# Optimization experiments

Measured on AMD Instinct MI355X. Metric: run time of the kernel, lower is better.

Reference implementation:

```python
import jax, jax.numpy as jnp
import numpy as np

N, C, T, V, K, COUT, H, DK, DV = 32, 64, 512, 25, 3, 64, 4, 16, 16
BN_EPS = 1e-5
LN_EPS = 1e-6


def setup_inputs() -> dict:
    key = jax.random.key(0)
    ks = jax.random.split(key, 8)
    s = jnp.float32(0.02)
    f32 = jnp.float32
    inp = {
        'x': jax.random.normal(ks[0], (N, C, T, V), f32),
        'A': jax.random.uniform(ks[1], (K, V, V), f32) / V,
        # BatchNorm2d(in_channels) -- eval mode params
        'bn1_g': jnp.ones((C,), f32), 'bn1_b': jnp.zeros((C,), f32),
        'bn1_m': jnp.zeros((C,), f32), 'bn1_v': jnp.ones((C,), f32),
        # partconv: Conv2d(C, COUT*K, kernel (1,1)) == pointwise
        'pconv_w': jax.random.normal(ks[2], (K * COUT, C), f32) * s,
        'pconv_b': jnp.zeros((K * COUT,), f32),
        # AdapGraphConv projections (stored as [d_in, d_out] for x @ W)
        'wq': jax.random.normal(ks[3], (C, H * DK), f32) * s,
        'wk': jax.random.normal(ks[4], (C, H * DK), f32) * s,
        'wv': jax.random.normal(ks[5], (C, H * DV), f32) * s,
        'fc_w': jax.random.normal(ks[6], (H * DV, COUT), f32) * s,
        'ln_g': jnp.ones((C,), f32), 'ln_b': jnp.zeros((C,), f32),
        # weighted-sum gate scalar
        'gate_w': jnp.float32(1.0),
        # SCN output BN
        'bn2_g': jnp.ones((COUT,), f32), 'bn2_b': jnp.zeros((COUT,), f32),
        'bn2_m': jnp.zeros((COUT,), f32), 'bn2_v': jnp.ones((COUT,), f32),
        # TCN: Conv2d(COUT, COUT, (9,1), padding (4,0))
        'tconv_w': jax.random.normal(ks[7], (COUT, COUT, 9, 1), f32) * s,
        'tconv_b': jnp.zeros((COUT,), f32),
        'bn3_g': jnp.ones((COUT,), f32), 'bn3_b': jnp.zeros((COUT,), f32),
        'bn3_m': jnp.zeros((COUT,), f32), 'bn3_v': jnp.ones((COUT,), f32),
    }
    return inp


def _bn(x, g, b, m, v):
    # eval-mode BatchNorm2d over channel axis 1 of NCHW
    sh = (1, -1, 1, 1)
    inv = g.reshape(sh) / jnp.sqrt(v.reshape(sh) + BN_EPS)
    return (x - m.reshape(sh)) * inv + b.reshape(sh)


def _block(x, A, bn1_g, bn1_b, bn1_m, bn1_v, pconv_w, pconv_b, wq, wk, wv,
           fc_w, ln_g, ln_b, gate_w, bn2_g, bn2_b, bn2_m, bn2_v,
           tconv_w, tconv_b, bn3_g, bn3_b, bn3_m, bn3_v):
    n, c, t, v = x.shape
    inp = _bn(x, bn1_g, bn1_b, bn1_m, bn1_v)                 # [N,C,T,V]
    # pointwise partconv then partition-wise graph aggregation
    f_c = jnp.einsum('nctv,oc->notv', inp, pconv_w) + pconv_b.reshape(1, -1, 1, 1)
    f_c = f_c.reshape(n, K, COUT, t, v)
    f_c = jnp.einsum('nkctv,kvw->nctw', f_c, A)              # [N,COUT,T,V]
    # AdapGraphConv over joints, batched across N*T
    fa = inp.transpose(0, 2, 3, 1).reshape(n * t, v, c)      # [NT,V,C]
    mu = fa.mean(-1, keepdims=True)
    var = fa.var(-1, keepdims=True)
    qn = (fa - mu) / jnp.sqrt(var + LN_EPS) * ln_g + ln_b    # LN on q only
    q = (qn @ wq).reshape(n * t, v, H, DK)
    k = (fa @ wk).reshape(n * t, v, H, DK)
    vv = (fa @ wv).reshape(n * t, v, H, DV)
    att = jnp.einsum('bqhd,bkhd->bhqk', q, k) / np.float32(np.sqrt(DK))
    att = jax.nn.softmax(att, axis=-1)                       # [NT,H,V,V]
    xh = jnp.einsum('bhqk,bkhd->bqhd', att, vv).reshape(n * t, v, H * DV)
    fa_out = xh @ fc_w + fa                                  # identity residual (C==COUT)
    fa_out = fa_out.reshape(n, t, v, COUT).transpose(0, 3, 1, 2)
    # gated fusion, BN + ReLU
    f = (fa_out * gate_w + f_c) * 0.5
    f = jax.nn.relu(_bn(f, bn2_g, bn2_b, bn2_m, bn2_v))
    # temporal conv (9,1), pad (4,0), then BN; dropout=0 => identity
    y = jax.lax.conv_general_dilated(
        f, tconv_w, window_strides=(1, 1), padding=((4, 4), (0, 0)),
        dimension_numbers=('NCHW', 'OIHW', 'NCHW'))
    y = y + tconv_b.reshape(1, -1, 1, 1)
    y = _bn(y, bn3_g, bn3_b, bn3_m, bn3_v)
    return jax.nn.relu(y + x)                                # identity block residual


def reference(x, A, bn1_g, bn1_b, bn1_m, bn1_v, pconv_w, pconv_b, wq, wk, wv,
              fc_w, ln_g, ln_b, gate_w, bn2_g, bn2_b, bn2_m, bn2_v,
              tconv_w, tconv_b, bn3_g, bn3_b, bn3_m, bn3_v):
    return _block(x, A, bn1_g, bn1_b, bn1_m, bn1_v, pconv_w, pconv_b, wq, wk,
                  wv, fc_w, ln_g, ln_b, gate_w, bn2_g, bn2_b, bn2_m, bn2_v,
                  tconv_w, tconv_b, bn3_g, bn3_b, bn3_m, bn3_v)
```

## Files before the change

### kernel.cpp

```cpp
#include <hip/hip_runtime.h>

#define NB   32
#define C    64
#define T    512
#define V    25
#define KP   3
#define CO   64
#define H    4
#define BN_EPS 1e-5f
#define LN_EPS 1e-6f

typedef float f32x4 __attribute__((ext_vector_type(4)));
typedef short bf16x8 __attribute__((ext_vector_type(8)));
typedef unsigned short u16;
typedef unsigned int u32;
typedef u32 u32x2 __attribute__((ext_vector_type(2)));
#define MFMA(a,b,c) __builtin_amdgcn_mfma_f32_16x16x32_bf16((a),(b),(c),0,0,0)

__device__ __forceinline__ u16 f2bf(float x) {
    union { float f; unsigned u; } v; v.f = x;
    unsigned r = (v.u + 0x7FFFu + ((v.u >> 16) & 1u)) >> 16;
    return (u16)r;
}
__device__ __forceinline__ float bf2f(u16 h) {
    union { unsigned u; float f; } v; v.u = ((unsigned)h) << 16;
    return v.f;
}
__device__ __forceinline__ u32x2 pack4(const f32x4& a) {
    u32x2 p;
    p[0] = (u32)f2bf(a[0]) | ((u32)f2bf(a[1]) << 16);
    p[1] = (u32)f2bf(a[2]) | ((u32)f2bf(a[3]) << 16);
    return p;
}

#define WOFF 52428800ull

__global__ __launch_bounds__(256) void prep_kernel(
    const float* __restrict__ A, const float* __restrict__ pconv_w,
    const float* __restrict__ pconv_b,
    const float* __restrict__ wq, const float* __restrict__ wk,
    const float* __restrict__ wv, const float* __restrict__ fc_w,
    const float* __restrict__ tconv_w, const float* __restrict__ tconv_b,
    const float* __restrict__ ln_g, const float* __restrict__ ln_b,
    const float* __restrict__ bn1_g, const float* __restrict__ bn1_b,
    const float* __restrict__ bn1_m, const float* __restrict__ bn1_v,
    const float* __restrict__ bn2_g, const float* __restrict__ bn2_b,
    const float* __restrict__ bn2_m, const float* __restrict__ bn2_v,
    const float* __restrict__ bn3_g, const float* __restrict__ bn3_b,
    const float* __restrict__ bn3_m, const float* __restrict__ bn3_v,
    u16* __restrict__ akt, u16* __restrict__ wp2,
    u16* __restrict__ wqt, u16* __restrict__ wkt, u16* __restrict__ wvt,
    u16* __restrict__ fct, float* __restrict__ bagg, u16* __restrict__ wtc,
    float* __restrict__ uvec, float* __restrict__ w0vec,
    float* __restrict__ bnc)
{
    const int stride = gridDim.x * 256;
    for (int i = blockIdx.x * 256 + threadIdx.x; i < 71296; i += stride) {
        if (i < 3840) {
            int k = i / 1280, r = i - k * 1280, w = r / 40, v = r - w * 40;
            float val = (w < V && v < V) ? A[k * V * V + v * V + w] : 0.f;
            akt[i] = f2bf(val);
        } else if (i < 16128) {
            int i2 = i - 3840;
            int c = i2 / 192, kk = i2 - c * 192, k = kk / 64, ci = kk - k * 64;
            wp2[i2] = f2bf(pconv_w[(k * 64 + c) * 64 + ci]);
        } else if (i < 20224) {
            int i2 = i - 16128; int j = i2 / 64, c = i2 - j * 64;
            wqt[i2] = f2bf(wq[c * 64 + j] * ln_g[c]);
        } else if (i < 24320) {
            int i2 = i - 20224; int j = i2 / 64, c = i2 - j * 64;
            wkt[i2] = f2bf(wk[c * 64 + j]);
        } else if (i < 28416) {
            int i2 = i - 24320; int j = i2 / 64, c = i2 - j * 64;
            wvt[i2] = f2bf(wv[c * 64 + j]);
        } else if (i < 32512) {
            int i2 = i - 28416; int c = i2 / 64, d = i2 - c * 64;
            fct[i2] = f2bf(fc_w[d * 64 + c]);
        } else if (i < 34112) {
            int i2 = i - 32512; int c = i2 / 25, w = i2 - c * 25;
            float s = 0.f;
            for (int k = 0; k < KP; ++k) {
                float cs = 0.f;
                for (int v = 0; v < V; ++v) cs += A[k * V * V + v * V + w];
                s += pconv_b[k * 64 + c] * cs;
            }
            bagg[i2] = s;
        } else if (i < 70976) {
            int i2 = i - 34112;
            int co = i2 / 576, rem = i2 - co * 576, dt = rem / 64, ci = rem - dt * 64;
            wtc[i2] = f2bf(tconv_w[(co * 64 + ci) * 9 + dt]);
        } else if (i < 71040) {
            int j = i - 70976; float s = 0.f;
            for (int c = 0; c < 64; ++c) s += ln_g[c] * wq[c * 64 + j];
            uvec[j] = s;
        } else if (i < 71104) {
            int j = i - 71040; float s = 0.f;
            for (int c = 0; c < 64; ++c) s += ln_b[c] * wq[c * 64 + j];
            w0vec[j] = s;
        } else if (i < 71168) {
            int c = i - 71104;
            float s1 = bn1_g[c] * rsqrtf(bn1_v[c] + BN_EPS);
            bnc[c]      = s1;
            bnc[64 + c] = bn1_b[c] - bn1_m[c] * s1;
        } else if (i < 71232) {
            int c = i - 71168;
            float s2 = bn2_g[c] * rsqrtf(bn2_v[c] + BN_EPS);
            bnc[128 + c] = s2;
            bnc[192 + c] = bn2_b[c] - bn2_m[c] * s2;
        } else {
            int c = i - 71232;
            float s3 = bn3_g[c] * rsqrtf(bn3_v[c] + BN_EPS);
            bnc[256 + c] = s3;
            bnc[320 + c] = tconv_b[c] * s3 + (bn3_b[c] - bn3_m[c] * s3);
        }
    }
}

#define OFF_INPV  0
#define OFF_XHT   0
#define OFF_INPT  5120
#define OFF_Q2    8720
#define OFF_ATT   8720
#define OFF_K2    15520
#define OFF_VVT   22320
#define OFF_LNS   27440
#define OFF_MU    29040
#define OFF_RSTD  29140
#define OFF_YT    29240
#define OFF_S     29240
#define LDS_BYTES 39640

#define LDSF(off) ((float*)(s_raw + (off)))
#define LDSH(off) ((u16*)(s_raw + (off)))
#define LDSV8(b)  (*(const bf16x8*)(s_raw + (b)))

__global__ __launch_bounds__(256) void scn_kernel(
    const float* __restrict__ x,
    const u16* __restrict__ akt, const u16* __restrict__ wp2,
    const u16* __restrict__ wqt, const u16* __restrict__ wkt,
    const u16* __restrict__ wvt, const u16* __restrict__ fct,
    const float* __restrict__ bagg,
    const float* __restrict__ uvec, const float* __restrict__ w0vec,
    const float* __restrict__ gate_w, const float* __restrict__ bnc,
    u16* __restrict__ f_out)
{
    const int nt   = blockIdx.x;
    const int n    = nt >> 9;
    const int t    = nt & 511;
    const int tid  = threadIdx.x;
    const int lane = tid & 63;
    const int wid  = tid >> 6;
    const int r0   = lane & 15;
    const int g    = lane >> 4;

    __shared__ __align__(16) unsigned char s_raw[LDS_BYTES];

    const float gate = gate_w[0];

    #pragma unroll
    for (int it = 0; it < 7; ++it) {
        int i = tid + it * 256;
        if (i < 1600) {
            int c = i / 25, v = i - c * 25;
            float f = x[((n * 64 + c) * 512 + t) * 25 + v] * bnc[c] + bnc[64 + c];
            u16 hb = f2bf(f);
            LDSH(OFF_INPV)[c * 40 + v] = hb;
            LDSH(OFF_INPT)[v * 72 + c] = hb;
        }
    }
    for (int i = tid; i < 960; i += 256) {
        int c = i / 15, vz = 25 + (i - c * 15);
        LDSH(OFF_INPV)[c * 40 + vz] = 0;
    }
    {
        bf16x8 z = {0,0,0,0,0,0,0,0};
        for (int i = tid; i < 1170; i += 256)
            *(bf16x8*)(s_raw + OFF_Q2 + i * 16) = z;
    }
    __syncthreads();

    #pragma unroll
    for (int ii = 0; ii < 6; ++ii) {
        int idx = wid * 6 + ii;
        int k = idx >> 3, rem = idx & 7, mt = rem >> 1, ntt = rem & 1;
        bf16x8 a = LDSV8(OFF_INPV + ((mt * 16 + r0) * 40 + g * 8) * 2);
        bf16x8 b = *(const bf16x8*)(&akt[(k * 32 + ntt * 16 + r0) * 40 + g * 8]);
        f32x4 acc = {0.f, 0.f, 0.f, 0.f};
        acc = MFMA(a, b, acc);
        int w = ntt * 16 + r0, cb = mt * 16 + g * 4;
        if (w < 25)
            *(u32x2*)&LDSH(OFF_YT)[w * 200 + k * 64 + cb] = pack4(acc);
    }
    #pragma unroll
    for (int ii = 0; ii < 2; ++ii) {
        int idx = wid * 2 + ii, mtj = idx >> 1, ntv = idx & 1;
        f32x4 acc = {0.f, 0.f, 0.f, 0.f};
        #pragma unroll
        for (int ks = 0; ks < 2; ++ks) {
            bf16x8 a = *(const bf16x8*)(&wkt[(mtj * 16 + r0) * 64 + ks * 32 + g * 8]);
            bf16x8 b = LDSV8(OFF_INPT + ((ntv * 16 + r0) * 72 + ks * 32 + g * 8) * 2);
            acc = MFMA(a, b, acc);
        }
        int v = ntv * 16 + r0;
        if (v < 25)
            *(u32x2*)&LDSH(OFF_K2)[v * 136 + mtj * 32 + g * 4] = pack4(acc);
    }
    #pragma unroll
    for (int ii = 0; ii < 2; ++ii) {
        int idx = wid * 2 + ii, mt = idx >> 2, ntt = idx & 3;
        f32x4 acc = {0.f, 0.f, 0.f, 0.f};
        #pragma unroll
        for (int ks = 0; ks < 2; ++ks) {
            bf16x8 a = LDSV8(OFF_INPT + ((mt * 16 + r0) * 72 + ks * 32 + g * 8) * 2);
            bf16x8 b = *(const bf16x8*)(&wvt[(ntt * 16 + r0) * 64 + ks * 32 + g * 8]);
            acc = MFMA(a, b, acc);
        }
        int j = ntt * 16 + r0;
        #pragma unroll
        for (int r = 0; r < 4; ++r) {
            int v = mt * 16 + g * 4 + r;
            if (v < 25) LDSH(OFF_VVT)[j * 40 + v] = f2bf(acc[r]);
        }
    }
    #pragma unroll
    for (int ii = 0; ii < 2; ++ii) {
        int idx = wid * 2 + ii, mtj = idx >> 1, ntv = idx & 1;
        f32x4 acc = {0.f, 0.f, 0.f, 0.f};
        #pragma unroll
        for (int ks = 0; ks < 2; ++ks) {
            bf16x8 a = *(const bf16x8*)(&wqt[(mtj * 16 + r0) * 64 + ks * 32 + g * 8]);
            bf16x8 b = LDSV8(OFF_INPT + ((ntv * 16 + r0) * 72 + ks * 32 + g * 8) * 2);
            acc = MFMA(a, b, acc);
        }
        int v = ntv * 16 + r0;
        if (v < 25)
            *(u32x2*)&LDSH(OFF_Q2)[v * 136 + mtj * 32 + g * 4] = pack4(acc);
    }
    if (tid < 200) {
        int v = tid >> 3, p = tid & 7;
        const u16* row = LDSH(OFF_INPT) + v * 72 + p * 8;
        float s1 = 0.f, s2 = 0.f;
        #pragma unroll
        for (int cc = 0; cc < 8; ++cc) {
            float xv = bf2f(row[cc]);
            s1 += xv; s2 += xv * xv;
        }
        LDSF(OFF_LNS)[(v * 8 + p) * 2]     = s1;
        LDSF(OFF_LNS)[(v * 8 + p) * 2 + 1] = s2;
    }
    __syncthreads();

    if (tid < 25) {
        float s1 = 0.f, s2 = 0.f;
        #pragma unroll
        for (int p = 0; p < 8; ++p) {
            s1 += LDSF(OFF_LNS)[(tid * 8 + p) * 2];
            s2 += LDSF(OFF_LNS)[(tid * 8 + p) * 2 + 1];
        }
        float mu = s1 * (1.f / 64.f);
        float var = s2 * (1.f / 64.f) - mu * mu;
        LDSF(OFF_MU)[tid]   = mu;
        LDSF(OFF_RSTD)[tid] = rsqrtf(var + LN_EPS);
    }
    __syncthreads();

    #pragma unroll
    for (int it = 0; it < 7; ++it) {
        int i = tid + it * 256;
        if (i < 1600) {
            int v = i >> 6, j = i & 63;
            int jo = (j >> 4) * 32 + (j & 15);
            float raw = bf2f(LDSH(OFF_Q2)[v * 136 + jo]);
            float rs = LDSF(OFF_RSTD)[v], m = LDSF(OFF_MU)[v];
            LDSH(OFF_Q2)[v * 136 + jo] =
                f2bf(0.25f * (rs * raw - rs * m * uvec[j] + w0vec[j]));
        }
    }
    f32x4 agg_reg[2];
    #pragma unroll
    for (int ii = 0; ii < 2; ++ii) {
        int idx = wid * 2 + ii, mt = idx >> 1, ntt = idx & 1;
        f32x4 acc = {0.f, 0.f, 0.f, 0.f};
        #pragma unroll
        for (int ks = 0; ks < 6; ++ks) {
            bf16x8 a = *(const bf16x8*)(&wp2[(mt * 16 + r0) * 192 + ks * 32 + g * 8]);
            int brow = ntt * 16 + r0; if (brow > 24) brow = 24;
            bf16x8 b = LDSV8(OFF_YT + (brow * 200 + ks * 32 + g * 8) * 2);
            acc = MFMA(a, b, acc);
        }
        int w = ntt * 16 + r0, cb = mt * 16 + g * 4;
        if (w < 25) {
            #pragma unroll
            for (int r = 0; r < 4; ++r) acc[r] += bagg[(cb + r) * 25 + w];
        }
        agg_reg[ii] = acc;
    }
    __syncthreads();

    #pragma unroll
    for (int ii = 0; ii < 4; ++ii) {
        int idx = wid * 4 + ii;
        int h = idx >> 2, mt = (idx >> 1) & 1, ntc = idx & 1;
        bf16x8 a = LDSV8(OFF_Q2 + ((mt * 16 + r0) * 136 + h * 32 + g * 8) * 2);
        bf16x8 b = LDSV8(OFF_K2 + ((ntc * 16 + r0) * 136 + h * 32 + g * 8) * 2);
        f32x4 acc = {0.f, 0.f, 0.f, 0.f};
        acc = MFMA(a, b, acc);
        int kv = ntc * 16 + r0;
        if (kv < 25) {
            #pragma unroll
            for (int r = 0; r < 4; ++r) {
                int qv = mt * 16 + g * 4 + r;
                if (qv < 25)
                    LDSF(OFF_S)[(h * 25 + qv) * 26 + kv] = acc[r];
            }
        }
    }
    __syncthreads();

    if (tid < 100) {
        int h = tid / 25, qv = tid - h * 25;
        const float* srow = LDSF(OFF_S) + (h * 25 + qv) * 26;
        float row[25]; float mx = -1e30f;
        #pragma unroll
        for (int kv = 0; kv < 25; ++kv) {
            float s = srow[kv];
            row[kv] = s; mx = fmaxf(mx, s);
        }
        float sum = 0.f;
        #pragma unroll
        for (int kv = 0; kv < 25; ++kv) { float e = __expf(row[kv] - mx); row[kv] = e; sum += e; }
        float inv = 1.f / sum;
        u16* arow = LDSH(OFF_ATT) + (h * 32 + qv) * 40;
        #pragma unroll
        for (int kv = 0; kv < 25; ++kv) arow[kv] = f2bf(row[kv] * inv);
        #pragma unroll
        for (int kv = 25; kv < 32; ++kv) arow[kv] = 0;
    }
    __syncthreads();

    #pragma unroll
    for (int ii = 0; ii < 2; ++ii) {
        int idx = wid * 2 + ii, h = idx >> 1, mt = idx & 1;
        bf16x8 a = LDSV8(OFF_ATT + ((h * 32 + mt * 16 + r0) * 40 + g * 8) * 2);
        bf16x8 b = LDSV8(OFF_VVT + ((h * 16 + r0) * 40 + g * 8) * 2);
        f32x4 acc = {0.f, 0.f, 0.f, 0.f};
        acc = MFMA(a, b, acc);
        #pragma unroll
        for (int r = 0; r < 4; ++r) {
            int v = mt * 16 + g * 4 + r;
            if (v < 25)
                LDSH(OFF_XHT)[v * 72 + h * 16 + r0] = f2bf(acc[r]);
        }
    }
    __syncthreads();

    #pragma unroll
    for (int ii = 0; ii < 2; ++ii) {
        int idx = wid * 2 + ii, mt = idx >> 1, ntt = idx & 1;
        f32x4 acc = {0.f, 0.f, 0.f, 0.f};
        #pragma unroll
        for (int ks = 0; ks < 2; ++ks) {
            bf16x8 a = *(const bf16x8*)(&fct[(mt * 16 + r0) * 64 + ks * 32 + g * 8]);
            bf16x8 b = LDSV8(OFF_XHT + ((ntt * 16 + r0) * 72 + ks * 32 + g * 8) * 2);
            acc = MFMA(a, b, acc);
        }
        int v = ntt * 16 + r0;
        if (v < 25) {
            int cb = mt * 16 + g * 4;
            u16 hh[4];
            #pragma unroll
            for (int r = 0; r < 4; ++r) {
                int c = cb + r;
                float fa_out = acc[r] + bf2f(LDSH(OFF_INPT)[v * 72 + c]);
                float fv = (fa_out * gate + agg_reg[ii][r]) * 0.5f;
                fv = fmaxf(fv * bnc[128 + c] + bnc[192 + c], 0.f);
                hh[r] = f2bf(fv);
            }
            u32x2 pk;
            pk[0] = (u32)hh[0] | ((u32)hh[1] << 16);
            pk[1] = (u32)hh[2] | ((u32)hh[3] << 16);
            *(u32x2*)&f_out[((n * 512 + t) * 25 + v) * 64 + cb] = pk;
        }
    }
}

#define FB_STRIDE 40

__global__ __launch_bounds__(256) void tcn_mfma(
    const u16* __restrict__ f, const float* __restrict__ x,
    const u16* __restrict__ wtc, const float* __restrict__ bnc,
    float* __restrict__ out)
{
    const int bid  = blockIdx.x;
    const int n    = bid >> 5;
    const int t0   = (bid & 31) * 16;
    const int tid  = threadIdx.x;
    const int lane = tid & 63;
    const int wid  = tid >> 6;
    const int r0   = lane & 15;
    const int g    = lane >> 4;
    const int co_base = wid * 16;

    __shared__ __align__(16) u16 s_fB[24 * 25 * FB_STRIDE];

    f32x4 acc[25];
    #pragma unroll
    for (int i = 0; i < 25; ++i) acc[i] = (f32x4){0.f, 0.f, 0.f, 0.f};

    for (int ph = 0; ph < 2; ++ph) {
        const int ci0 = ph * 32;
        __syncthreads();
        for (int u = tid; u < 2400; u += 256) {
            int q = u & 3, rv = u >> 2;
            int tp = rv / 25, v = rv - tp * 25;
            int tg = t0 + tp - 4;
            bf16x8 val = {0,0,0,0,0,0,0,0};
            if (tg >= 0 && tg < 512)
                val = *(const bf16x8*)&f[((n * 512 + tg) * 25 + v) * 64 + ci0 + q * 8];
            *(bf16x8*)&s_fB[rv * FB_STRIDE + q * 8] = val;
        }
        __syncthreads();

        bf16x8 aF[9];
        #pragma unroll
        for (int dt = 0; dt < 9; ++dt)
            aF[dt] = *(const bf16x8*)(&wtc[((co_base + r0) * 9 + dt) * 64 + ci0 + g * 8]);

        #pragma unroll
        for (int nt2 = 0; nt2 < 25; ++nt2) {
            int c0 = nt2 * 16 + r0;
            int tb = c0 / 25, v = c0 - tb * 25;
            #pragma unroll
            for (int dt = 0; dt < 9; ++dt) {
                bf16x8 bF = *(const bf16x8*)(&s_fB[((tb + dt) * 25 + v) * FB_STRIDE + g * 8]);
                acc[nt2] = MFMA(aF[dt], bF, acc[nt2]);
            }
        }
    }

    float s3v[4], pre[4];
    #pragma unroll
    for (int r = 0; r < 4; ++r) {
        int co = co_base + g * 4 + r;
        s3v[r] = bnc[256 + co];
        pre[r] = bnc[320 + co];
    }
    #pragma unroll
    for (int nt2 = 0; nt2 < 25; ++nt2) {
        int c0 = nt2 * 16 + r0;
        int tb = c0 / 25, v = c0 - tb * 25;
        #pragma unroll
        for (int r = 0; r < 4; ++r) {
            int co = co_base + g * 4 + r;
            int idx = ((n * 64 + co) * 512 + t0 + tb) * 25 + v;
            float y = acc[nt2][r] * s3v[r] + pre[r] + x[idx];
            out[idx] = fmaxf(y, 0.f);
        }
    }
}

extern "C" void kernel_launch(void* const* d_in, const int* in_sizes, int n_in,
                              void* d_out, int out_size, void* d_ws, size_t ws_size,
                              hipStream_t stream) {
    const float* x       = (const float*)d_in[0];
    const float* A       = (const float*)d_in[1];
    const float* bn1_g   = (const float*)d_in[2];
    const float* bn1_b   = (const float*)d_in[3];
    const float* bn1_m   = (const float*)d_in[4];
    const float* bn1_v   = (const float*)d_in[5];
    const float* pconv_w = (const float*)d_in[6];
    const float* pconv_b = (const float*)d_in[7];
    const float* wq      = (const float*)d_in[8];
    const float* wk      = (const float*)d_in[9];
    const float* wv      = (const float*)d_in[10];
    const float* fc_w    = (const float*)d_in[11];
    const float* ln_g    = (const float*)d_in[12];
    const float* ln_b    = (const float*)d_in[13];
    const float* gate_w  = (const float*)d_in[14];
    const float* bn2_g   = (const float*)d_in[15];
    const float* bn2_b   = (const float*)d_in[16];
    const float* bn2_m   = (const float*)d_in[17];
    const float* bn2_v   = (const float*)d_in[18];
    const float* tconv_w = (const float*)d_in[19];
    const float* tconv_b = (const float*)d_in[20];
    const float* bn3_g   = (const float*)d_in[21];
    const float* bn3_b   = (const float*)d_in[22];
    const float* bn3_m   = (const float*)d_in[23];
    const float* bn3_v   = (const float*)d_in[24];

    char* ws = (char*)d_ws;
    u16*   f_bf  = (u16*)ws;
    u16*   akt   = (u16*)(ws + WOFF);
    u16*   wp2   = (u16*)(ws + WOFF + 7680);
    u16*   wqt   = (u16*)(ws + WOFF + 32256);
    u16*   wkt   = (u16*)(ws + WOFF + 40448);
    u16*   wvt   = (u16*)(ws + WOFF + 48640);
    u16*   fct   = (u16*)(ws + WOFF + 56832);
    float* bagg  = (float*)(ws + WOFF + 65024);
    u16*   wtc   = (u16*)(ws + WOFF + 71424);
    float* uvec  = (float*)(ws + WOFF + 145152);
    float* w0vec = (float*)(ws + WOFF + 145408);
    float* bnc   = (float*)(ws + WOFF + 145664);
    float* outp  = (float*)d_out;

    prep_kernel<<<dim3(64), dim3(256), 0, stream>>>(
        A, pconv_w, pconv_b, wq, wk, wv, fc_w, tconv_w, tconv_b, ln_g, ln_b,
        bn1_g, bn1_b, bn1_m, bn1_v, bn2_g, bn2_b, bn2_m, bn2_v,
        bn3_g, bn3_b, bn3_m, bn3_v,
        akt, wp2, wqt, wkt, wvt, fct, bagg, wtc, uvec, w0vec, bnc);
    scn_kernel<<<dim3(NB * T), dim3(256), 0, stream>>>(
        x, akt, wp2, wqt, wkt, wvt, fct, bagg, uvec, w0vec, gate_w, bnc, f_bf);
    tcn_mfma<<<dim3(NB * 32), dim3(256), 0, stream>>>(
        f_bf, x, wtc, bnc, outp);
}
```

Before: 324.1 us.

## Fuse attention softmax into MFMA registers with wave shuffles, drop barriers

Each wave now computes the QK^T score tiles for its own head and keeps them in registers. The row max and row sum are found with xor-shuffles across the 16 lanes instead of writing scores to LDS and running a 100-thread serial softmax. Because the wave that writes the attention probabilities is the same wave that reads them in the following AV MFMA, two __syncthreads and the fp32 score round trip through LDS are removed. The cost is extra shuffle and exp work per lane, and the probability buffer moves to a region that overlaps the earlier YT scratch area.

After: 349.3 us. 1.08x slower.

```diff
diff --git a/kernel.cpp b/kernel.cpp
--- a/kernel.cpp
+++ b/kernel.cpp
@@ -120,14 +120,13 @@
 #define OFF_XHT   0
 #define OFF_INPT  5120
 #define OFF_Q2    8720
-#define OFF_ATT   8720
 #define OFF_K2    15520
 #define OFF_VVT   22320
 #define OFF_LNS   27440
 #define OFF_MU    29040
 #define OFF_RSTD  29140
 #define OFF_YT    29240
-#define OFF_S     29240
+#define OFF_ATT2  29248
 #define LDS_BYTES 39640
 
 #define LDSF(off) ((float*)(s_raw + (off)))
@@ -297,51 +296,48 @@
     }
     __syncthreads();
 
-    #pragma unroll
-    for (int ii = 0; ii < 4; ++ii) {
-        int idx = wid * 4 + ii;
-        int h = idx >> 2, mt = (idx >> 1) & 1, ntc = idx & 1;
-        bf16x8 a = LDSV8(OFF_Q2 + ((mt * 16 + r0) * 136 + h * 32 + g * 8) * 2);
-        bf16x8 b = LDSV8(OFF_K2 + ((ntc * 16 + r0) * 136 + h * 32 + g * 8) * 2);
-        f32x4 acc = {0.f, 0.f, 0.f, 0.f};
-        acc = MFMA(a, b, acc);
-        int kv = ntc * 16 + r0;
-        if (kv < 25) {
+    {
+        const int h = wid;
+        f32x4 accT[4];
+        #pragma unroll
+        for (int ii = 0; ii < 4; ++ii) {
+            int mt = ii >> 1, ntc = ii & 1;
+            bf16x8 a = LDSV8(OFF_Q2 + ((mt * 16 + r0) * 136 + h * 32 + g * 8) * 2);
+            bf16x8 b = LDSV8(OFF_K2 + ((ntc * 16 + r0) * 136 + h * 32 + g * 8) * 2);
+            f32x4 z4 = {0.f, 0.f, 0.f, 0.f};
+            accT[ii] = MFMA(a, b, z4);
+        }
+        #pragma unroll
+        for (int mt = 0; mt < 2; ++mt) {
             #pragma unroll
             for (int r = 0; r < 4; ++r) {
+                float a0 = accT[mt * 2 + 0][r];
+                float a1v = accT[mt * 2 + 1][r];
+                float mx = fmaxf(a0, (r0 < 9) ? a1v : -1e30f);
+                #pragma unroll
+                for (int msk = 1; msk <= 8; msk <<= 1)
+                    mx = fmaxf(mx, __shfl_xor(mx, msk, 64));
+                float e0 = __expf(a0 - mx);
+                float e1 = (r0 < 9) ? __expf(a1v - mx) : 0.f;
+                float sm = e0 + e1;
+                #pragma unroll
+                for (int msk = 1; msk <= 8; msk <<= 1)
+                    sm += __shfl_xor(sm, msk, 64);
+                float inv = 1.f / sm;
                 int qv = mt * 16 + g * 4 + r;
-                if (qv < 25)
-                    LDSF(OFF_S)[(h * 25 + qv) * 26 + kv] = acc[r];
+                if (qv < 25) {
+                    u16* arow = LDSH(OFF_ATT2) + (h * 32 + qv) * 40;
+                    arow[r0]      = f2bf(e0 * inv);
+                    arow[16 + r0] = (r0 < 9) ? f2bf(e1 * inv) : (u16)0;
+                }
             }
         }
     }
-    __syncthreads();
-
-    if (tid < 100) {
-        int h = tid / 25, qv = tid - h * 25;
-        const float* srow = LDSF(OFF_S) + (h * 25 + qv) * 26;
-        float row[25]; float mx = -1e30f;
-        #pragma unroll
-        for (int kv = 0; kv < 25; ++kv) {
-            float s = srow[kv];
-            row[kv] = s; mx = fmaxf(mx, s);
-        }
-        float sum = 0.f;
-        #pragma unroll
-        for (int kv = 0; kv < 25; ++kv) { float e = __expf(row[kv] - mx); row[kv] = e; sum += e; }
-        float inv = 1.f / sum;
-        u16* arow = LDSH(OFF_ATT) + (h * 32 + qv) * 40;
-        #pragma unroll
-        for (int kv = 0; kv < 25; ++kv) arow[kv] = f2bf(row[kv] * inv);
-        #pragma unroll
-        for (int kv = 25; kv < 32; ++kv) arow[kv] = 0;
-    }
-    __syncthreads();
 
     #pragma unroll
     for (int ii = 0; ii < 2; ++ii) {
         int idx = wid * 2 + ii, h = idx >> 1, mt = idx & 1;
-        bf16x8 a = LDSV8(OFF_ATT + ((h * 32 + mt * 16 + r0) * 40 + g * 8) * 2);
+        bf16x8 a = LDSV8(OFF_ATT2 + ((h * 32 + mt * 16 + r0) * 40 + g * 8) * 2);
         bf16x8 b = LDSV8(OFF_VVT + ((h * 16 + r0) * 40 + g * 8) * 2);
         f32x4 acc = {0.f, 0.f, 0.f, 0.f};
         acc = MFMA(a, b, acc);
```
